# Performance work log

Hardware: AMD Instinct MI355X
Metric: run time of the kernel (lower is better)

Reference implementation:

```python
import jax, jax.numpy as jnp
import numpy as np

EPS_VAR = 1e-10
EPS_PERP = 1e-07


def setup_inputs() -> dict:
    key = jax.random.key(0)
    k1, k2 = jax.random.split(key, 2)
    bs, dim_z, W, H, K = 64, 64, 32, 32, 1024
    z_from_encoder = jax.random.normal(k1, (bs, dim_z, W, H), dtype=jnp.float32)
    codebook = jax.random.normal(k2, (K, dim_z), dtype=jnp.float32)
    var_q = jnp.ones((1,), dtype=jnp.float32)
    return {"z_from_encoder": z_from_encoder, "var_q": var_q, "codebook": codebook}


def _vq_forward(z_from_encoder, var_q, codebook):
    bs, dim_z, W, H = z_from_encoder.shape
    K = codebook.shape[0]
    # precision = 1 / clamp(var_q, min=1e-10); gaussian_1 -> global scalar weight
    precision_q = 1.0 / jnp.clip(var_q, EPS_VAR)
    weight = (0.5 * precision_q).reshape(())  # scalar

    # [bs, dim_z, W, H] -> [N, dim_z], N = bs*W*H
    z_flat = jnp.transpose(z_from_encoder, (0, 2, 3, 1)).reshape(-1, dim_z)

    # squared euclidean distance to every code: ||z||^2 + ||c||^2 - 2 z c^T  -> [N, K]
    d2 = (jnp.sum(z_flat * z_flat, axis=1, keepdims=True)
          + jnp.sum(codebook * codebook, axis=1)
          - 2.0 * (z_flat @ codebook.T))
    logit = -(weight * d2)

    log_probs = jax.nn.log_softmax(logit, axis=-1)   # [N, K]
    probs = jnp.exp(log_probs)                        # [N, K]

    # deterministic quantization: argmax -> gather codebook (== one_hot @ codebook)
    indices = jnp.argmax(logit, axis=1)               # [N]
    z_q = codebook[indices].reshape(bs, W, H, dim_z)
    z_to_decoder = jnp.transpose(z_q, (0, 3, 1, 2))   # [bs, dim_z, W, H]

    # avg_probs = mean of hard one-hot encodings (histogram of code usage)
    N = indices.shape[0]
    avg_probs = jnp.zeros((K,), dtype=logit.dtype).at[indices].add(1.0) / N

    # kld_discrete = sum(probs * log_probs) / bs  (sum over N and K)
    kld_discrete = jnp.sum(probs * log_probs) / bs
    # kld_continuous = mean over batch of sum_i weight * (z - z_q)^2
    diff2 = (z_from_encoder - z_to_decoder) ** 2
    kld_continuous = jnp.mean(jnp.sum(weight * diff2, axis=(1, 2, 3)))
    loss = kld_discrete + kld_continuous

    perplexity = jnp.exp(-jnp.sum(avg_probs * jnp.log(avg_probs + EPS_PERP)))
    return z_to_decoder, loss, perplexity


def reference(z_from_encoder, var_q, codebook):
    return _vq_forward(z_from_encoder, var_q, codebook)
```

## Files before the change

kernel.cpp:

```cpp
#include <hip/hip_runtime.h>

#define WS_CNORM_B  512
#define WS_COUNTS_B 4608
#define WS_CBHI_B   8704
#define WS_CBLO_B   139776
#define WS_ZERO_B   8704

typedef __attribute__((ext_vector_type(8))) short short8;
typedef __attribute__((ext_vector_type(4))) float f32x4;

__device__ __forceinline__ unsigned short f2bf(float x) {
  unsigned u = __builtin_bit_cast(unsigned, x);
  u += 0x7fffu + ((u >> 16) & 1u);
  return (unsigned short)(u >> 16);
}
__device__ __forceinline__ float bf2f(unsigned short h) {
  unsigned u = ((unsigned)h) << 16;
  return __builtin_bit_cast(float, u);
}
__device__ __forceinline__ int qw(int r, int d) {
  return (r << 6) | (d ^ (r & 31));
}

__global__ __launch_bounds__(256) void vq_prep(const float* __restrict__ cb,
                                               char* __restrict__ ws) {
  int tid = blockIdx.x * 256 + threadIdx.x;
  int k = tid >> 6, d = threadIdx.x & 63;
  float v = cb[tid];
  unsigned short hi = f2bf(v);
  unsigned short lo = f2bf(v - bf2f(hi));
  ((unsigned short*)(ws + WS_CBHI_B))[tid] = hi;
  ((unsigned short*)(ws + WS_CBLO_B))[tid] = lo;
  float s = v * v;
  #pragma unroll
  for (int o = 32; o > 0; o >>= 1) s += __shfl_down(s, o);
  if (d == 0) ((float*)(ws + WS_CNORM_B))[k] = s;
}

#define ST_OFF   32768
#define FIDX_OFF 34048

__global__ __launch_bounds__(256, 4) void vq_main(const float* __restrict__ z,
                                                  const float* __restrict__ cb,
                                                  const float* __restrict__ var_q,
                                                  char* __restrict__ ws,
                                                  float* __restrict__ out) {
  __shared__ __align__(16) char smem[34304];

  const int t = threadIdx.x;
  const int b = blockIdx.x;
  const int bb = b >> 4, p0 = (b & 15) << 6;
  const int l = t & 63, wv = t >> 6;
  const int lg = l >> 4, lr = l & 15;
  const float w = 0.5f / fmaxf(var_q[0], 1e-10f);
  const float w2 = 2.f * w;
  const float nw = -w;

  for (int i = 0; i < 8; ++i) {
    int idx = t + i * 256;
    int d2 = idx >> 6, p = idx & 63;
    float v0 = z[bb * 65536 + (2 * d2) * 1024 + p0 + p];
    float v1 = z[bb * 65536 + (2 * d2 + 1) * 1024 + p0 + p];
    unsigned short h0 = f2bf(v0), h1 = f2bf(v1);
    unsigned short o0 = f2bf(v0 - bf2f(h0)), o1 = f2bf(v1 - bf2f(h1));
    int byte = (p * 128 + d2 * 4) ^ ((p & 7) << 4);
    *(unsigned*)(smem + byte) = ((unsigned)h1 << 16) | h0;
    *(unsigned*)(smem + 8192 + byte) = ((unsigned)o1 << 16) | o0;
  }
  __syncthreads();

  short8 a_hi[2], a_lo[2];
  {
    int row = wv * 16 + lr;
    #pragma unroll
    for (int ks = 0; ks < 2; ++ks) {
      int byte = (row * 128 + ks * 64 + lg * 16) ^ ((row & 7) << 4);
      a_hi[ks] = *(const short8*)(smem + byte);
      a_lo[ks] = *(const short8*)(smem + 8192 + byte);
    }
  }
  __syncthreads();

  const char* cbh = ws + WS_CBHI_B;
  const char* cbl = ws + WS_CBLO_B;
  {
    #pragma unroll
    for (int pas = 0; pas < 2; ++pas) {
      int o = t + pas * 256;
      int dst = (o * 16) ^ (((o >> 3) & 7) << 4);
      *(f32x4*)(smem + dst) = *(const f32x4*)(cbh + o * 16);
      *(f32x4*)(smem + 8192 + dst) = *(const f32x4*)(cbl + o * 16);
    }
  }
  __syncthreads();

  float m[4], S1[4], S2[4], b1[4], b2[4];
  #pragma unroll
  for (int j = 0; j < 4; ++j) {
    m[j] = -1e30f; S1[j] = 0.f; S2[j] = 0.f; b1[j] = -1e30f; b2[j] = -1e30f;
  }

  const float* cnf = (const float*)(ws + WS_CNORM_B);

  for (int ch = 0; ch < 16; ++ch) {
    char* cur = smem + (ch & 1) * 16384;
    char* nxt = smem + ((ch + 1) & 1) * 16384;
    f32x4 rh0, rh1, rl0, rl1;
    const bool pf = ch < 15;
    if (pf) {
      const char* sh = cbh + (ch + 1) * 8192 + t * 16;
      const char* sl = cbl + (ch + 1) * 8192 + t * 16;
      rh0 = *(const f32x4*)sh;  rh1 = *(const f32x4*)(sh + 4096);
      rl0 = *(const f32x4*)sl;  rl1 = *(const f32x4*)(sl + 4096);
    }
    float cn2[4];
    #pragma unroll
    for (int ct = 0; ct < 4; ++ct) cn2[ct] = nw * cnf[ch * 64 + ct * 16 + lr];

    f32x4 acc[4];
    #pragma unroll
    for (int ct = 0; ct < 4; ++ct) {
      f32x4 a = {};
      #pragma unroll
      for (int ks = 0; ks < 2; ++ks) {
        int cr = ct * 16 + lr;
        int byte = (cr * 128 + ks * 64 + lg * 16) ^ ((cr & 7) << 4);
        short8 bh = *(const short8*)(cur + byte);
        a = __builtin_amdgcn_mfma_f32_16x16x32_bf16(a_hi[ks], bh, a, 0, 0, 0);
      }
      acc[ct] = a;
    }

    #pragma unroll
    for (int j = 0; j < 4; ++j) {
      float lv[4];
      #pragma unroll
      for (int ct = 0; ct < 4; ++ct) lv[ct] = fmaf(acc[ct][j], w2, cn2[ct]);
      float lm = fmaxf(fmaxf(lv[0], lv[1]), fmaxf(lv[2], lv[3]));
      float mn = fmaxf(m[j], lm);
      float sc = __expf(m[j] - mn);
      S1[j] *= sc; S2[j] *= sc; m[j] = mn;
      #pragma unroll
      for (int ct = 0; ct < 4; ++ct) {
        float x = lv[ct];
        unsigned ku = (unsigned)(ch * 64 + ct * 16 + lr);
        unsigned xb = (__builtin_bit_cast(unsigned, x) & ~1023u) | ku;
        float xp = __builtin_bit_cast(float, xb);
        float tm = fminf(b1[j], xp);
        b1[j] = fmaxf(b1[j], xp);
        b2[j] = fmaxf(b2[j], tm);
        float e = __expf(x - mn);
        S1[j] += e;
        S2[j] = fmaf(x, e, S2[j]);
      }
    }

    if (pf) {
      #pragma unroll
      for (int pas = 0; pas < 2; ++pas) {
        int o = t + pas * 256;
        int dst = (o * 16) ^ (((o >> 3) & 7) << 4);
        *(f32x4*)(nxt + dst) = pas ? rh1 : rh0;
        *(f32x4*)(nxt + 8192 + dst) = pas ? rl1 : rl0;
      }
    }
    __syncthreads();
  }

  #pragma unroll
  for (int st = 1; st < 16; st <<= 1) {
    #pragma unroll
    for (int j = 0; j < 4; ++j) {
      float om = __shfl_xor(m[j], st);
      float o1 = __shfl_xor(S1[j], st);
      float o2 = __shfl_xor(S2[j], st);
      float ov1 = __shfl_xor(b1[j], st);
      float ov2 = __shfl_xor(b2[j], st);
      float mn = fmaxf(m[j], om);
      float sa = __expf(m[j] - mn), sb = __expf(om - mn);
      S1[j] = sa * S1[j] + sb * o1;
      S2[j] = sa * S2[j] + sb * o2;
      m[j] = mn;
      float nb1 = fmaxf(b1[j], ov1);
      float nb2 = fmaxf(fminf(b1[j], ov1), fmaxf(b2[j], ov2));
      b1[j] = nb1; b2[j] = nb2;
    }
  }

  float* stw = (float*)(smem + ST_OFF);
  if (lr == 0) {
    #pragma unroll
    for (int j = 0; j < 4; ++j) {
      int r = wv * 16 + lg * 4 + j;
      float* p = stw + r * 5;
      p[0] = m[j]; p[1] = S1[j]; p[2] = S2[j]; p[3] = b1[j]; p[4] = b2[j];
    }
  }
  __syncthreads();

  int* fidx = (int*)(smem + FIDX_OFF);
  float rowent = 0.f, d2min = 0.f;
  if (t < 64) {
    const float* p = stw + t * 5;
    float mn = p[0], s1 = p[1], s2 = p[2];
    int ka = (int)(__builtin_bit_cast(unsigned, p[3]) & 1023u);
    int kb = (int)(__builtin_bit_cast(unsigned, p[4]) & 1023u);
    rowent = (s2 - mn * s1) / s1 - __logf(s1);
    const float* zp = z + bb * 65536 + p0 + t;
    const float* c1p = cb + ka * 64;
    const float* c2p = cb + kb * 64;
    float zn = 0.f, d1 = 0.f, d2 = 0.f;
    #pragma unroll 4
    for (int d4 = 0; d4 < 16; ++d4) {
      f32x4 ca = *(const f32x4*)(c1p + d4 * 4);
      f32x4 cc = *(const f32x4*)(c2p + d4 * 4);
      #pragma unroll
      for (int e = 0; e < 4; ++e) {
        float v = zp[(d4 * 4 + e) * 1024];
        zn = fmaf(v, v, zn);
        d1 = fmaf(v, ca[e], d1);
        d2 = fmaf(v, cc[e], d2);
      }
    }
    float da = zn + cnf[ka] - 2.f * d1;
    float db = zn + cnf[kb] - 2.f * d2;
    int kwin; float dwin;
    if (da < db || (da == db && ka < kb)) { kwin = ka; dwin = da; }
    else { kwin = kb; dwin = db; }
    fidx[t] = kwin;
    d2min = dwin;
    atomicAdd((unsigned*)(ws + WS_COUNTS_B) + kwin, 1u);
  }
  #pragma unroll
  for (int o = 32; o > 0; o >>= 1) {
    rowent += __shfl_down(rowent, o);
    d2min += __shfl_down(d2min, o);
  }
  if (t == 0) {
    float* wsf = (float*)ws;
    int slot = b & 63;
    atomicAdd(&wsf[slot * 2], rowent);
    atomicAdd(&wsf[slot * 2 + 1], d2min);
  }
  __syncthreads();

  float* zl = (float*)smem;
  for (int i = 0; i < 16; ++i) {
    int idx = t + i * 256;
    int r = idx >> 6, d = idx & 63;
    zl[qw(r, d)] = cb[fidx[r] * 64 + d];
  }
  __syncthreads();
  float* outz = out + bb * 65536 + p0;
  #pragma unroll
  for (int i = 0; i < 4; ++i) {
    int q = t + i * 256;
    int d = q >> 4, rq = q & 15, r = rq << 2;
    f32x4 v;
    v.x = zl[qw(r + 0, d)];
    v.y = zl[qw(r + 1, d)];
    v.z = zl[qw(r + 2, d)];
    v.w = zl[qw(r + 3, d)];
    *(f32x4*)&outz[d * 1024 + r] = v;
  }
}

__global__ __launch_bounds__(1024) void vq_finalize(const float* __restrict__ var_q,
                                                    char* __restrict__ ws,
                                                    float* __restrict__ out) {
  __shared__ float red[48];
  int t = threadIdx.x;
  const unsigned* counts = (const unsigned*)(ws + WS_COUNTS_B);
  const float* wsf = (const float*)ws;
  float avg = (float)counts[t] * (1.0f / 65536.0f);
  float term = avg * __logf(avg + 1e-7f);
  float pd = 0.f, pc = 0.f;
  if (t < 64) { pd = wsf[2 * t]; pc = wsf[2 * t + 1]; }
  #pragma unroll
  for (int o = 32; o > 0; o >>= 1) {
    term += __shfl_down(term, o);
    pd += __shfl_down(pd, o);
    pc += __shfl_down(pc, o);
  }
  int wv = t >> 6, lane = t & 63;
  if (lane == 0) { red[wv * 3] = term; red[wv * 3 + 1] = pd; red[wv * 3 + 2] = pc; }
  __syncthreads();
  if (t == 0) {
    float ts = 0.f, ps = 0.f, cs = 0.f;
    #pragma unroll
    for (int i = 0; i < 16; ++i) {
      ts += red[i * 3]; ps += red[i * 3 + 1]; cs += red[i * 3 + 2];
    }
    float w = 0.5f / fmaxf(var_q[0], 1e-10f);
    out[4194304] = ps / 64.f + w * cs / 64.f;
    out[4194305] = __expf(-ts);
  }
}

extern "C" void kernel_launch(void* const* d_in, const int* in_sizes, int n_in,
                              void* d_out, int out_size, void* d_ws, size_t ws_size,
                              hipStream_t stream) {
  const float* z = (const float*)d_in[0];
  const float* vq = (const float*)d_in[1];
  const float* cb = (const float*)d_in[2];
  float* out = (float*)d_out;
  char* ws = (char*)d_ws;

  hipMemsetAsync(d_ws, 0, WS_ZERO_B, stream);
  vq_prep<<<256, 256, 0, stream>>>(cb, ws);
  vq_main<<<1024, 256, 0, stream>>>(z, cb, vq, ws, out);
  vq_finalize<<<1, 1024, 0, stream>>>(vq, ws, out);
}
```

Measured before the change: 71.74 us.

## Load codebook fragments directly from global into registers, drop LDS double buffering

Each wave now reads its bf16 codebook MFMA operands straight from global memory (L2-resident) into registers, replacing the double-buffered LDS staging and the per-chunk __syncthreads. It also drops the hi/lo bf16 split of the codebook and z, which was computed but unused in the MFMA path, shrinking LDS use and prep work. This removes barriers and LDS traffic. In exchange, every wave redundantly fetches the codebook from global/L2, and global load latency is exposed, with only a 2-way unroll to hide it.

```diff
diff --git a/kernel.cpp b/kernel.cpp
--- a/kernel.cpp
+++ b/kernel.cpp
@@ -3,7 +3,6 @@
 #define WS_CNORM_B  512
 #define WS_COUNTS_B 4608
 #define WS_CBHI_B   8704
-#define WS_CBLO_B   139776
 #define WS_ZERO_B   8704
 
 typedef __attribute__((ext_vector_type(8))) short short8;
@@ -14,10 +13,6 @@
   u += 0x7fffu + ((u >> 16) & 1u);
   return (unsigned short)(u >> 16);
 }
-__device__ __forceinline__ float bf2f(unsigned short h) {
-  unsigned u = ((unsigned)h) << 16;
-  return __builtin_bit_cast(float, u);
-}
 __device__ __forceinline__ int qw(int r, int d) {
   return (r << 6) | (d ^ (r & 31));
 }
@@ -25,27 +20,24 @@
 __global__ __launch_bounds__(256) void vq_prep(const float* __restrict__ cb,
                                                char* __restrict__ ws) {
   int tid = blockIdx.x * 256 + threadIdx.x;
-  int k = tid >> 6, d = threadIdx.x & 63;
+  int k = tid >> 6;
   float v = cb[tid];
-  unsigned short hi = f2bf(v);
-  unsigned short lo = f2bf(v - bf2f(hi));
-  ((unsigned short*)(ws + WS_CBHI_B))[tid] = hi;
-  ((unsigned short*)(ws + WS_CBLO_B))[tid] = lo;
+  ((unsigned short*)(ws + WS_CBHI_B))[tid] = f2bf(v);
   float s = v * v;
   #pragma unroll
   for (int o = 32; o > 0; o >>= 1) s += __shfl_down(s, o);
-  if (d == 0) ((float*)(ws + WS_CNORM_B))[k] = s;
-}
-
-#define ST_OFF   32768
-#define FIDX_OFF 34048
+  if ((threadIdx.x & 63) == 0) ((float*)(ws + WS_CNORM_B))[k] = s;
+}
+
+#define ST_OFF   16384
+#define FIDX_OFF 17664
 
 __global__ __launch_bounds__(256, 4) void vq_main(const float* __restrict__ z,
                                                   const float* __restrict__ cb,
                                                   const float* __restrict__ var_q,
                                                   char* __restrict__ ws,
                                                   float* __restrict__ out) {
-  __shared__ __align__(16) char smem[34304];
+  __shared__ __align__(16) char smem[17920];
 
   const int t = threadIdx.x;
   const int b = blockIdx.x;
@@ -62,37 +54,20 @@
     float v0 = z[bb * 65536 + (2 * d2) * 1024 + p0 + p];
     float v1 = z[bb * 65536 + (2 * d2 + 1) * 1024 + p0 + p];
     unsigned short h0 = f2bf(v0), h1 = f2bf(v1);
-    unsigned short o0 = f2bf(v0 - bf2f(h0)), o1 = f2bf(v1 - bf2f(h1));
     int byte = (p * 128 + d2 * 4) ^ ((p & 7) << 4);
     *(unsigned*)(smem + byte) = ((unsigned)h1 << 16) | h0;
-    *(unsigned*)(smem + 8192 + byte) = ((unsigned)o1 << 16) | o0;
-  }
-  __syncthreads();
-
-  short8 a_hi[2], a_lo[2];
+  }
+  __syncthreads();
+
+  short8 a_hi[2];
   {
     int row = wv * 16 + lr;
     #pragma unroll
     for (int ks = 0; ks < 2; ++ks) {
       int byte = (row * 128 + ks * 64 + lg * 16) ^ ((row & 7) << 4);
       a_hi[ks] = *(const short8*)(smem + byte);
-      a_lo[ks] = *(const short8*)(smem + 8192 + byte);
-    }
-  }
-  __syncthreads();
-
-  const char* cbh = ws + WS_CBHI_B;
-  const char* cbl = ws + WS_CBLO_B;
-  {
-    #pragma unroll
-    for (int pas = 0; pas < 2; ++pas) {
-      int o = t + pas * 256;
-      int dst = (o * 16) ^ (((o >> 3) & 7) << 4);
-      *(f32x4*)(smem + dst) = *(const f32x4*)(cbh + o * 16);
-      *(f32x4*)(smem + 8192 + dst) = *(const f32x4*)(cbl + o * 16);
-    }
-  }
-  __syncthreads();
+    }
+  }
 
   float m[4], S1[4], S2[4], b1[4], b2[4];
   #pragma unroll
@@ -101,18 +76,17 @@
   }
 
   const float* cnf = (const float*)(ws + WS_CNORM_B);
-
+  const char* bp = ws + WS_CBHI_B + lr * 128 + lg * 16;
+
+  #pragma unroll 2
   for (int ch = 0; ch < 16; ++ch) {
-    char* cur = smem + (ch & 1) * 16384;
-    char* nxt = smem + ((ch + 1) & 1) * 16384;
-    f32x4 rh0, rh1, rl0, rl1;
-    const bool pf = ch < 15;
-    if (pf) {
-      const char* sh = cbh + (ch + 1) * 8192 + t * 16;
-      const char* sl = cbl + (ch + 1) * 8192 + t * 16;
-      rh0 = *(const f32x4*)sh;  rh1 = *(const f32x4*)(sh + 4096);
-      rl0 = *(const f32x4*)sl;  rl1 = *(const f32x4*)(sl + 4096);
-    }
+    short8 bv[4][2];
+    #pragma unroll
+    for (int ct = 0; ct < 4; ++ct)
+      #pragma unroll
+      for (int ks = 0; ks < 2; ++ks)
+        bv[ct][ks] = *(const short8*)(bp + ch * 8192 + ct * 2048 + ks * 64);
+
     float cn2[4];
     #pragma unroll
     for (int ct = 0; ct < 4; ++ct) cn2[ct] = nw * cnf[ch * 64 + ct * 16 + lr];
@@ -121,13 +95,8 @@
     #pragma unroll
     for (int ct = 0; ct < 4; ++ct) {
       f32x4 a = {};
-      #pragma unroll
-      for (int ks = 0; ks < 2; ++ks) {
-        int cr = ct * 16 + lr;
-        int byte = (cr * 128 + ks * 64 + lg * 16) ^ ((cr & 7) << 4);
-        short8 bh = *(const short8*)(cur + byte);
-        a = __builtin_amdgcn_mfma_f32_16x16x32_bf16(a_hi[ks], bh, a, 0, 0, 0);
-      }
+      a = __builtin_amdgcn_mfma_f32_16x16x32_bf16(a_hi[0], bv[ct][0], a, 0, 0, 0);
+      a = __builtin_amdgcn_mfma_f32_16x16x32_bf16(a_hi[1], bv[ct][1], a, 0, 0, 0);
       acc[ct] = a;
     }
 
@@ -154,17 +123,6 @@
         S2[j] = fmaf(x, e, S2[j]);
       }
     }
-
-    if (pf) {
-      #pragma unroll
-      for (int pas = 0; pas < 2; ++pas) {
-        int o = t + pas * 256;
-        int dst = (o * 16) ^ (((o >> 3) & 7) << 4);
-        *(f32x4*)(nxt + dst) = pas ? rh1 : rh0;
-        *(f32x4*)(nxt + 8192 + dst) = pas ? rl1 : rl0;
-      }
-    }
-    __syncthreads();
   }
 
   #pragma unroll
```

After: 97.82 us. 1.36x slower.
